# Kernel optimization log

Hardware: AMD Instinct MI355X
Metric: run time of the kernel (lower is better)

The kernel has to match this reference:

```python
import jax, jax.numpy as jnp
import numpy as np

KD_T = 4.0
PATCH_NUM = 64
MASK_NUM = 8
BATCH = 256
DIM = 2048
P = PATCH_NUM - MASK_NUM  # 56


def setup_inputs() -> dict:
    key = jax.random.key(0)
    k1, k2, k3 = jax.random.split(key, 3)
    ebg = jax.random.normal(k1, (BATCH, DIM), dtype=jnp.float32)
    ebp = jax.random.normal(k2, (P * BATCH, DIM), dtype=jnp.float32)
    labels = jax.random.randint(k3, (BATCH,), 0, 10, dtype=jnp.int64)
    return {"ebg": ebg, "ebp": ebp, "labels": labels}


def _kl(y_s, y_t, T):
    # Faithful to KLDiv with dim=0 on vectors: softmax over the feature axis,
    # F.kl_div(..., reduction='batchmean') on a length-D vector divides by D.
    D = y_s.shape[-1]
    log_p_s = jax.nn.log_softmax(y_s / T, axis=-1)
    log_p_t = jax.nn.log_softmax(y_t / T, axis=-1)
    p_t = jnp.exp(log_p_t)
    return jnp.sum(p_t * (log_p_t - log_p_s), axis=-1) * (T * T / D)


def reference(ebg, ebp, labels):
    sg = jax.lax.stop_gradient
    ebp_r = ebp.reshape(P, BATCH, DIM)          # [P, B, D]
    ebp_bar = ebp_r.mean(axis=0)                # [B, D]

    # soft_dil_loss: sum over batch of symmetric KD with detached targets
    soft_dil = jnp.sum(_kl(ebg, sg(ebp_bar), KD_T)) + jnp.sum(_kl(ebp_bar, sg(ebg), KD_T))

    # soft_dcl_loss: per (batch, patch) pair on squared differences
    ebp_t = jnp.transpose(ebp_r, (1, 0, 2))     # [B, P, D]
    dg = (ebg[:, None, :] - ebp_t) ** 2         # [B, P, D]
    db = (ebp_bar[:, None, :] - ebp_t) ** 2     # [B, P, D]
    soft_dcl = (jnp.sum(_kl(dg, db, KD_T)) + jnp.sum(_kl(db, dg, KD_T))) / P

    return (soft_dil, soft_dcl)
```

## Files before the change

### kernel.cpp

```cpp
#include <hip/hip_runtime.h>
#include <math.h>

#define DIM    2048
#define BATCH  256
#define PN     56
#define CHUNK  128
#define NCHUNK 4
#define NQ     4
#define QCOLS  (CHUNK * NCHUNK)
#define NBLK   (BATCH * NQ)
constexpr float KD_T = 4.0f;

__device__ __forceinline__ float wave_sum(float v) {
#pragma unroll
    for (int o = 32; o > 0; o >>= 1) v += __shfl_xor(v, o, 64);
    return v;
}
__device__ __forceinline__ float half_sum(float v) {
#pragma unroll
    for (int o = 16; o > 0; o >>= 1) v += __shfl_xor(v, o, 64);
    return v;
}
__device__ __forceinline__ double wave_sum_d(double v) {
#pragma unroll
    for (int o = 32; o > 0; o >>= 1) v += __shfl_xor(v, o, 64);
    return v;
}

__global__ void __launch_bounds__(256) fused_kernel(const float* __restrict__ ebg,
                                                    const float* __restrict__ ebp,
                                                    float* __restrict__ pdcl,
                                                    float* __restrict__ pdil)
{
    __shared__ float  ebp_s[PN * CHUNK];
    __shared__ float4 redbar[4][32];
    __shared__ float  bar_s[CHUNK];
    __shared__ float  redl[4][4];

    const int t    = threadIdx.x;
    const int lane = t & 63;
    const int wv   = t >> 6;
    const int sub  = lane >> 5;
    const int c32  = lane & 31;
    const int bid  = blockIdx.x;
    const int b    = bid >> 2;
    const int q    = bid & (NQ - 1);
    const float invT = 1.0f / KD_T;

    const size_t rowoff = (size_t)b * DIM + (size_t)q * QCOLS;

    float acc[7][4];
#pragma unroll
    for (int j = 0; j < 7; ++j)
#pragma unroll
        for (int k = 0; k < 4; ++k) acc[j][k] = 0.f;

    float dss = 0.f, dts = 0.f, dt1 = 0.f, dt2 = 0.f;

    for (int c = 0; c < NCHUNK; ++c) {
        const size_t cb = rowoff + (size_t)c * CHUNK;

        const int prow0 = t >> 5;
        const int cc4   = (t & 31) * 4;
        float4 vals[7];
#pragma unroll
        for (int it = 0; it < 7; ++it) {
            const int p = it * 8 + prow0;
            vals[it] = *(const float4*)(ebp + (size_t)p * (BATCH * DIM) + cb + cc4);
        }
        float4 bp = {0.f, 0.f, 0.f, 0.f};
#pragma unroll
        for (int it = 0; it < 7; ++it) {
            const int p = it * 8 + prow0;
            *(float4*)(ebp_s + p * CHUNK + cc4) = vals[it];
            bp.x += vals[it].x; bp.y += vals[it].y;
            bp.z += vals[it].z; bp.w += vals[it].w;
        }
        bp.x += __shfl_xor(bp.x, 32, 64);
        bp.y += __shfl_xor(bp.y, 32, 64);
        bp.z += __shfl_xor(bp.z, 32, 64);
        bp.w += __shfl_xor(bp.w, 32, 64);
        if (c32 == lane) ;
        if (lane < 32) redbar[wv][lane] = bp;
        __syncthreads();
        if (t < 32) {
            float4 s0 = redbar[0][t], s1 = redbar[1][t],
                   s2 = redbar[2][t], s3 = redbar[3][t];
            float4 s;
            s.x = (s0.x + s1.x + s2.x + s3.x) * (1.0f / PN);
            s.y = (s0.y + s1.y + s2.y + s3.y) * (1.0f / PN);
            s.z = (s0.z + s1.z + s2.z + s3.z) * (1.0f / PN);
            s.w = (s0.w + s1.w + s2.w + s3.w) * (1.0f / PN);
            *(float4*)(bar_s + t * 4) = s;
        }
        __syncthreads();

        if (t < CHUNK) {
            float g = ebg[cb + t];
            float m = bar_s[t];
            float s = g * invT, tv = m * invT;
            float es = __expf(s), et = __expf(tv);
            float dd = tv - s;
            dss += es; dts += et;
            dt1 = fmaf(es, dd, dt1);
            dt2 = fmaf(et, dd, dt2);
        }

        const float4 g4 = *(const float4*)(ebg + cb + c32 * 4);
        const float4 m4 = *(const float4*)(bar_s + c32 * 4);
        const float gs[4] = {g4.x, g4.y, g4.z, g4.w};
        const float ms[4] = {m4.x, m4.y, m4.z, m4.w};
#pragma unroll
        for (int j = 0; j < 7; ++j) {
            const int row = wv * 14 + 2 * j + sub;
            float4 e = *(const float4*)(ebp_s + row * CHUNK + c32 * 4);
            float es_[4] = {e.x, e.y, e.z, e.w};
#pragma unroll
            for (int k = 0; k < 4; ++k) {
                float dg = gs[k] - es_[k];
                float db = ms[k] - es_[k];
                float a  = dg * dg * invT;
                float cc = db * db * invT;
                float ea = __expf(a), ec = __expf(cc);
                float d  = cc - a;
                acc[j][0] += ea;
                acc[j][1] += ec;
                acc[j][2] = fmaf(ea, d, acc[j][2]);
                acc[j][3] = fmaf(ec, d, acc[j][3]);
            }
        }
        __syncthreads();
    }

#pragma unroll
    for (int j = 0; j < 7; ++j) {
        float a0 = half_sum(acc[j][0]);
        float a1 = half_sum(acc[j][1]);
        float a2 = half_sum(acc[j][2]);
        float a3 = half_sum(acc[j][3]);
        if (c32 == 0) {
            const int row = wv * 14 + 2 * j + sub;
            float* qp = pdcl + (((size_t)row * BATCH + b) * NQ + q) * 4;
            qp[0] = a0; qp[1] = a1; qp[2] = a2; qp[3] = a3;
        }
    }
    dss = wave_sum(dss); dts = wave_sum(dts);
    dt1 = wave_sum(dt1); dt2 = wave_sum(dt2);
    if (lane == 0) { redl[wv][0] = dss; redl[wv][1] = dts; redl[wv][2] = dt1; redl[wv][3] = dt2; }
    __syncthreads();
    if (t == 0) {
        float* qp = pdil + (size_t)bid * 4;
#pragma unroll
        for (int k = 0; k < 4; ++k)
            qp[k] = redl[0][k] + redl[1][k] + redl[2][k] + redl[3][k];
    }
}

__global__ void __launch_bounds__(256) finalize1_kernel(const float* __restrict__ pdcl,
                                                        double* __restrict__ partial)
{
    __shared__ double sd[4];
    const int p = blockIdx.x, t = threadIdx.x, lane = t & 63, wv = t >> 6;
    const float* base = pdcl + ((size_t)p * BATCH + t) * NQ * 4;
    double A = 0.0, C = 0.0, T1 = 0.0, T2 = 0.0;
#pragma unroll
    for (int qq = 0; qq < NQ; ++qq) {
        float4 v = *(const float4*)(base + qq * 4);
        A += v.x; C += v.y; T1 += v.z; T2 += v.w;
    }
    double r = T2 / C - T1 / A;
    r = wave_sum_d(r);
    if (lane == 0) sd[wv] = r;
    __syncthreads();
    if (t == 0) partial[p] = sd[0] + sd[1] + sd[2] + sd[3];
}

__global__ void __launch_bounds__(256) finalize2_kernel(const double* __restrict__ partial,
                                                        const float* __restrict__ pdil,
                                                        float* __restrict__ out)
{
    __shared__ double sdc[4], sdl[4];
    const int t = threadIdx.x, lane = t & 63, wv = t >> 6;

    double vd = (t < PN) ? partial[t] : 0.0;

    const float* base = pdil + (size_t)t * NQ * 4;
    double ss = 0.0, ts = 0.0, u1 = 0.0, u2 = 0.0;
#pragma unroll
    for (int qq = 0; qq < NQ; ++qq) {
        float4 v = *(const float4*)(base + qq * 4);
        ss += v.x; ts += v.y; u1 += v.z; u2 += v.w;
    }
    double vl = u2 / ts - u1 / ss;

    vd = wave_sum_d(vd); vl = wave_sum_d(vl);
    if (lane == 0) { sdc[wv] = vd; sdl[wv] = vl; }
    __syncthreads();
    if (t == 0) {
        const double kT2 = (double)KD_T * KD_T;
        out[0] = (float)((sdl[0] + sdl[1] + sdl[2] + sdl[3]) * (kT2 / DIM));
        out[1] = (float)((sdc[0] + sdc[1] + sdc[2] + sdc[3]) * (kT2 / DIM / PN));
    }
}

extern "C" void kernel_launch(void* const* d_in, const int* in_sizes, int n_in,
                              void* d_out, int out_size, void* d_ws, size_t ws_size,
                              hipStream_t stream) {
    const float* ebg = (const float*)d_in[0];
    const float* ebp = (const float*)d_in[1];

    float*  pdcl    = (float*)d_ws;
    float*  pdil    = pdcl + (size_t)PN * BATCH * NQ * 4;
    double* partial = (double*)(pdil + (size_t)NBLK * 4);

    fused_kernel<<<NBLK, 256, 0, stream>>>(ebg, ebp, pdcl, pdil);
    finalize1_kernel<<<PN, 256, 0, stream>>>(pdcl, partial);
    finalize2_kernel<<<1, 256, 0, stream>>>(partial, pdil, (float*)d_out);
}
```

Measured before the change: 183.7 us.

## Prefetch next chunk into registers and drop the bar_s sync stage

Splits the chunk loop into load and process steps with double-buffered register arrays, so the global loads for the next chunk are issued while the current chunk is computed. Each thread now forms the patch mean directly from the redbar partial sums instead of a separate bar_s pass, which removes one __syncthreads per chunk. It also sets launch_bounds to a minimum of 4 blocks per CU. The extra 28 prefetch registers plus the occupancy hint could cause register spills or reduce occupancy.

```diff
diff --git a/kernel.cpp b/kernel.cpp
--- a/kernel.cpp
+++ b/kernel.cpp
@@ -27,14 +27,13 @@
     return v;
 }
 
-__global__ void __launch_bounds__(256) fused_kernel(const float* __restrict__ ebg,
-                                                    const float* __restrict__ ebp,
-                                                    float* __restrict__ pdcl,
-                                                    float* __restrict__ pdil)
+__global__ void __launch_bounds__(256, 4) fused_kernel(const float* __restrict__ ebg,
+                                                       const float* __restrict__ ebp,
+                                                       float* __restrict__ pdcl,
+                                                       float* __restrict__ pdil)
 {
     __shared__ float  ebp_s[PN * CHUNK];
     __shared__ float4 redbar[4][32];
-    __shared__ float  bar_s[CHUNK];
     __shared__ float  redl[4][4];
 
     const int t    = threadIdx.x;
@@ -46,8 +45,11 @@
     const int b    = bid >> 2;
     const int q    = bid & (NQ - 1);
     const float invT = 1.0f / KD_T;
+    const float invP = 1.0f / PN;
 
     const size_t rowoff = (size_t)b * DIM + (size_t)q * QCOLS;
+    const int prow0 = t >> 5;
+    const int cc4   = (t & 31) * 4;
 
     float acc[7][4];
 #pragma unroll
@@ -57,48 +59,43 @@
 
     float dss = 0.f, dts = 0.f, dt1 = 0.f, dt2 = 0.f;
 
-    for (int c = 0; c < NCHUNK; ++c) {
+    auto load_chunk = [&](int c, float4 v[7]) {
         const size_t cb = rowoff + (size_t)c * CHUNK;
-
-        const int prow0 = t >> 5;
-        const int cc4   = (t & 31) * 4;
-        float4 vals[7];
+#pragma unroll
+        for (int it = 0; it < 7; ++it)
+            v[it] = *(const float4*)(ebp + (size_t)(it * 8 + prow0) * (BATCH * DIM) + cb + cc4);
+    };
+
+    auto process = [&](int c, float4 v[7], float4 vn[7], bool more) {
+        const size_t cb = rowoff + (size_t)c * CHUNK;
+
+        float4 bp = {0.f, 0.f, 0.f, 0.f};
 #pragma unroll
         for (int it = 0; it < 7; ++it) {
-            const int p = it * 8 + prow0;
-            vals[it] = *(const float4*)(ebp + (size_t)p * (BATCH * DIM) + cb + cc4);
-        }
-        float4 bp = {0.f, 0.f, 0.f, 0.f};
-#pragma unroll
-        for (int it = 0; it < 7; ++it) {
-            const int p = it * 8 + prow0;
-            *(float4*)(ebp_s + p * CHUNK + cc4) = vals[it];
-            bp.x += vals[it].x; bp.y += vals[it].y;
-            bp.z += vals[it].z; bp.w += vals[it].w;
+            *(float4*)(ebp_s + (it * 8 + prow0) * CHUNK + cc4) = v[it];
+            bp.x += v[it].x; bp.y += v[it].y; bp.z += v[it].z; bp.w += v[it].w;
         }
         bp.x += __shfl_xor(bp.x, 32, 64);
         bp.y += __shfl_xor(bp.y, 32, 64);
         bp.z += __shfl_xor(bp.z, 32, 64);
         bp.w += __shfl_xor(bp.w, 32, 64);
-        if (c32 == lane) ;
         if (lane < 32) redbar[wv][lane] = bp;
         __syncthreads();
-        if (t < 32) {
-            float4 s0 = redbar[0][t], s1 = redbar[1][t],
-                   s2 = redbar[2][t], s3 = redbar[3][t];
-            float4 s;
-            s.x = (s0.x + s1.x + s2.x + s3.x) * (1.0f / PN);
-            s.y = (s0.y + s1.y + s2.y + s3.y) * (1.0f / PN);
-            s.z = (s0.z + s1.z + s2.z + s3.z) * (1.0f / PN);
-            s.w = (s0.w + s1.w + s2.w + s3.w) * (1.0f / PN);
-            *(float4*)(bar_s + t * 4) = s;
-        }
-        __syncthreads();
+
+        if (more) load_chunk(c + 1, vn);
+
+        float4 r0 = redbar[0][c32], r1 = redbar[1][c32],
+               r2 = redbar[2][c32], r3 = redbar[3][c32];
+        const float ms[4] = {(r0.x + r1.x + r2.x + r3.x) * invP,
+                             (r0.y + r1.y + r2.y + r3.y) * invP,
+                             (r0.z + r1.z + r2.z + r3.z) * invP,
+                             (r0.w + r1.w + r2.w + r3.w) * invP};
 
         if (t < CHUNK) {
+            const float* rb = (const float*)redbar;
+            float bc = (rb[t] + rb[128 + t] + rb[256 + t] + rb[384 + t]) * invP;
             float g = ebg[cb + t];
-            float m = bar_s[t];
-            float s = g * invT, tv = m * invT;
+            float s = g * invT, tv = bc * invT;
             float es = __expf(s), et = __expf(tv);
             float dd = tv - s;
             dss += es; dts += et;
@@ -107,9 +104,7 @@
         }
 
         const float4 g4 = *(const float4*)(ebg + cb + c32 * 4);
-        const float4 m4 = *(const float4*)(bar_s + c32 * 4);
         const float gs[4] = {g4.x, g4.y, g4.z, g4.w};
-        const float ms[4] = {m4.x, m4.y, m4.z, m4.w};
 #pragma unroll
         for (int j = 0; j < 7; ++j) {
             const int row = wv * 14 + 2 * j + sub;
@@ -120,9 +115,9 @@
                 float dg = gs[k] - es_[k];
                 float db = ms[k] - es_[k];
                 float a  = dg * dg * invT;
-                float cc = db * db * invT;
-                float ea = __expf(a), ec = __expf(cc);
-                float d  = cc - a;
+                float cc2 = db * db * invT;
+                float ea = __expf(a), ec = __expf(cc2);
+                float d  = cc2 - a;
                 acc[j][0] += ea;
                 acc[j][1] += ec;
                 acc[j][2] = fmaf(ea, d, acc[j][2]);
@@ -130,7 +125,14 @@
             }
         }
         __syncthreads();
-    }
+    };
+
+    float4 va[7], vb[7];
+    load_chunk(0, va);
+    process(0, va, vb, true);
+    process(1, vb, va, true);
+    process(2, va, vb, true);
+    process(3, vb, va, false);
 
 #pragma unroll
     for (int j = 0; j < 7; ++j) {
```

New measurement: 245.6 us. 1.34x slower.
